# Optimization experiments

Measured on AMD Instinct MI355X. Metric: run time of the kernel, lower is better.

The kernel has to match this reference:

```python
import jax, jax.numpy as jnp
import numpy as np

EPS = 1e-12  # matches tf.math.l2_normalize epsilon used by K.l2_normalize


def setup_inputs() -> dict:
    key = jax.random.key(0)
    k1, k2, k3 = jax.random.split(key, 3)
    B, N, C = 512, 256, 256
    x = jax.random.normal(k1, (B, N, C), dtype=jnp.float32)
    kernel = jax.random.normal(k2, (N, 1), dtype=jnp.float32)
    bias = jax.random.normal(k3, (N,), dtype=jnp.float32)
    return {"x": x, "kernel": kernel, "bias": bias}


def reference(x, kernel, bias):
    # x: [B, N, C]; kernel: [N, 1]; bias: [N]
    N = x.shape[-2]
    mid = N // 2
    # self-similarity: [B, N, N]
    sim = jnp.einsum('bnc,bmc->bnm', x, x)
    # l2-normalize along last axis (tf semantics: x * rsqrt(max(sum(x^2), eps)))
    coe = sim * jax.lax.rsqrt(jnp.maximum(jnp.sum(sim * sim, axis=-1, keepdims=True), EPS))
    # center row scaled by kernel: [B, N, 1]
    coe0 = coe[:, mid, :][..., None] * kernel
    # gating logits: [B, N, 1]
    w = jnp.einsum('bnm,bmk->bnk', coe, coe0) + bias[None, :, None]
    # softmax over spatial axis N, broadcast-multiply with input
    return jax.nn.softmax(w, axis=-2) * x
```

## Files before the change

### kernel.cpp

```cpp
#include <hip/hip_runtime.h>

#define B_N 256
#define B_C 256
#define MID 128

typedef float f32x4 __attribute__((ext_vector_type(4)));
typedef __bf16 bf16x8 __attribute__((ext_vector_type(8)));
typedef short short8 __attribute__((ext_vector_type(8)));

__device__ __forceinline__ unsigned short f2bf(float f) {
  unsigned int u = __builtin_bit_cast(unsigned int, f);
  u += 0x7fffu + ((u >> 16) & 1u);
  return (unsigned short)(u >> 16);
}

__device__ __forceinline__ float bf2f(unsigned short h) {
  return __builtin_bit_cast(float, (unsigned int)h << 16);
}

__global__ __launch_bounds__(512, 2) void spat_attn(
    const float* __restrict__ x, const float* __restrict__ kern,
    const float* __restrict__ bias, float* __restrict__ out)
{
  __shared__ __align__(16) unsigned short Xs[B_N * B_C];
  __shared__ float smid[B_N];
  __shared__ float r2s[B_N];
  __shared__ float vb[B_N];
  __shared__ float wlog[B_N];
  __shared__ float wexp[B_N];

  const int b = blockIdx.x;
  const int tid = threadIdx.x;
  const float* __restrict__ xb = x + (size_t)b * (B_N * B_C);

  #pragma unroll 4
  for (int i = 0; i < 16; ++i) {
    const int e8 = i * 4096 + tid * 8;
    const float4 f0 = *reinterpret_cast<const float4*>(xb + e8);
    const float4 f1 = *reinterpret_cast<const float4*>(xb + e8 + 4);
    const int r = e8 >> 8;
    const int q = (e8 >> 3) & 31;
    union { unsigned short us[8]; short8 v; } P;
    P.us[0] = f2bf(f0.x); P.us[1] = f2bf(f0.y); P.us[2] = f2bf(f0.z); P.us[3] = f2bf(f0.w);
    P.us[4] = f2bf(f1.x); P.us[5] = f2bf(f1.y); P.us[6] = f2bf(f1.z); P.us[7] = f2bf(f1.w);
    *reinterpret_cast<short8*>(&Xs[(r << 8) + ((q ^ (r & 7)) << 3)]) = P.v;
  }
  __syncthreads();

  const int w  = tid >> 6;
  const int l  = tid & 63;
  const int lr = l & 15;
  const int g  = l >> 4;
  const int sw = lr & 7;

  f32x4 acc[16][2];
  #pragma unroll
  for (int t = 0; t < 16; ++t) {
    acc[t][0] = {0.f, 0.f, 0.f, 0.f};
    acc[t][1] = {0.f, 0.f, 0.f, 0.f};
  }

  const int rb0 = 32 * w + lr;
  const int rb1 = rb0 + 16;
  #pragma unroll
  for (int kk = 0; kk < 8; ++kk) {
    const int q  = 4 * kk + g;
    const int qs = ((q ^ sw) << 3);
    const bf16x8 b0 = __builtin_bit_cast(bf16x8,
        *reinterpret_cast<const short8*>(&Xs[(rb0 << 8) + qs]));
    const bf16x8 b1 = __builtin_bit_cast(bf16x8,
        *reinterpret_cast<const short8*>(&Xs[(rb1 << 8) + qs]));
    #pragma unroll
    for (int t = 0; t < 16; ++t) {
      const bf16x8 a = __builtin_bit_cast(bf16x8,
          *reinterpret_cast<const short8*>(&Xs[((16 * t + lr) << 8) + qs]));
      acc[t][0] = __builtin_amdgcn_mfma_f32_16x16x32_bf16(a, b0, acc[t][0], 0, 0, 0);
      acc[t][1] = __builtin_amdgcn_mfma_f32_16x16x32_bf16(a, b1, acc[t][1], 0, 0, 0);
    }
  }

  float rp0 = 0.f, rp1 = 0.f;
  #pragma unroll
  for (int t = 0; t < 16; ++t) {
    #pragma unroll
    for (int r = 0; r < 4; ++r) {
      rp0 += acc[t][0][r] * acc[t][0][r];
      rp1 += acc[t][1][r] * acc[t][1][r];
    }
  }
  rp0 += __shfl_xor(rp0, 16); rp0 += __shfl_xor(rp0, 32);
  rp1 += __shfl_xor(rp1, 16); rp1 += __shfl_xor(rp1, 32);
  if (l < 16) {
    r2s[32 * w + l]      = rp0;
    r2s[32 * w + 16 + l] = rp1;
    smid[32 * w + l]      = acc[8][0][0];
    smid[32 * w + 16 + l] = acc[8][1][0];
  }
  __syncthreads();

  if (tid < B_N) {
    const float rinvm = rsqrtf(fmaxf(r2s[MID], 1e-12f));
    vb[tid] = smid[tid] * rinvm * kern[tid];
  }
  __syncthreads();

  float up0 = 0.f, up1 = 0.f;
  #pragma unroll
  for (int t = 0; t < 16; ++t) {
    #pragma unroll
    for (int r = 0; r < 4; ++r) {
      const float vv = vb[16 * t + 4 * g + r];
      up0 += acc[t][0][r] * vv;
      up1 += acc[t][1][r] * vv;
    }
  }
  up0 += __shfl_xor(up0, 16); up0 += __shfl_xor(up0, 32);
  up1 += __shfl_xor(up1, 16); up1 += __shfl_xor(up1, 32);
  if (l < 16) {
    const int n0 = 32 * w + l, n1 = n0 + 16;
    wlog[n0] = up0 * rsqrtf(fmaxf(r2s[n0], 1e-12f)) + bias[n0];
    wlog[n1] = up1 * rsqrtf(fmaxf(r2s[n1], 1e-12f)) + bias[n1];
  }
  __syncthreads();

  if (tid < 64) {
    const float a0 = wlog[tid], a1 = wlog[tid + 64], a2 = wlog[tid + 128], a3 = wlog[tid + 192];
    float mx = fmaxf(fmaxf(a0, a1), fmaxf(a2, a3));
    #pragma unroll
    for (int off = 32; off >= 1; off >>= 1) mx = fmaxf(mx, __shfl_xor(mx, off));
    const float e0 = __expf(a0 - mx), e1 = __expf(a1 - mx), e2 = __expf(a2 - mx), e3 = __expf(a3 - mx);
    float s = e0 + e1 + e2 + e3;
    #pragma unroll
    for (int off = 32; off >= 1; off >>= 1) s += __shfl_xor(s, off);
    const float inv = 1.0f / s;
    wexp[tid] = e0 * inv; wexp[tid + 64] = e1 * inv;
    wexp[tid + 128] = e2 * inv; wexp[tid + 192] = e3 * inv;
  }
  __syncthreads();

  float* __restrict__ ob = out + (size_t)b * (B_N * B_C);
  #pragma unroll 4
  for (int i = 0; i < 16; ++i) {
    const int e8 = i * 4096 + tid * 8;
    const int r = e8 >> 8;
    const int q = (e8 >> 3) & 31;
    union { short8 v; unsigned short us[8]; } P;
    P.v = *reinterpret_cast<const short8*>(&Xs[(r << 8) + ((q ^ (r & 7)) << 3)]);
    const float wt = wexp[r];
    float4 o0, o1;
    o0.x = bf2f(P.us[0]) * wt; o0.y = bf2f(P.us[1]) * wt;
    o0.z = bf2f(P.us[2]) * wt; o0.w = bf2f(P.us[3]) * wt;
    o1.x = bf2f(P.us[4]) * wt; o1.y = bf2f(P.us[5]) * wt;
    o1.z = bf2f(P.us[6]) * wt; o1.w = bf2f(P.us[7]) * wt;
    *reinterpret_cast<float4*>(ob + e8)     = o0;
    *reinterpret_cast<float4*>(ob + e8 + 4) = o1;
  }
}

extern "C" void kernel_launch(void* const* d_in, const int* in_sizes, int n_in,
                              void* d_out, int out_size, void* d_ws, size_t ws_size,
                              hipStream_t stream) {
  const float* x    = (const float*)d_in[0];
  const float* kern = (const float*)d_in[1];
  const float* bias = (const float*)d_in[2];
  float* out = (float*)d_out;
  const int nb = in_sizes[0] / (B_N * B_C);
  spat_attn<<<dim3(nb), dim3(512), 0, stream>>>(x, kern, bias, out);
}
```

Before: 64.63 us.

## Process two batches per block and prefetch the second into registers

The grid is halved so each block handles two batch items. The second item's input is loaded into registers while the first item's output is stored, so the global load overlaps the store phase. Output stores become nontemporal and the bf16 conversion now uses the builtin cast. Each thread holds 32 extra float4 prefetch registers, which risks spills or lower occupancy under the 512x2 launch bound, and halving the grid to 256 blocks may leave compute units idle.

```diff
diff --git a/kernel.cpp b/kernel.cpp
--- a/kernel.cpp
+++ b/kernel.cpp
@@ -3,50 +3,34 @@
 #define B_N 256
 #define B_C 256
 #define MID 128
+#define NELEM (B_N * B_C)
 
 typedef float f32x4 __attribute__((ext_vector_type(4)));
 typedef __bf16 bf16x8 __attribute__((ext_vector_type(8)));
 typedef short short8 __attribute__((ext_vector_type(8)));
 
-__device__ __forceinline__ unsigned short f2bf(float f) {
-  unsigned int u = __builtin_bit_cast(unsigned int, f);
-  u += 0x7fffu + ((u >> 16) & 1u);
-  return (unsigned short)(u >> 16);
-}
-
 __device__ __forceinline__ float bf2f(unsigned short h) {
   return __builtin_bit_cast(float, (unsigned int)h << 16);
 }
 
-__global__ __launch_bounds__(512, 2) void spat_attn(
-    const float* __restrict__ x, const float* __restrict__ kern,
-    const float* __restrict__ bias, float* __restrict__ out)
-{
-  __shared__ __align__(16) unsigned short Xs[B_N * B_C];
-  __shared__ float smid[B_N];
-  __shared__ float r2s[B_N];
-  __shared__ float vb[B_N];
-  __shared__ float wlog[B_N];
-  __shared__ float wexp[B_N];
-
-  const int b = blockIdx.x;
-  const int tid = threadIdx.x;
-  const float* __restrict__ xb = x + (size_t)b * (B_N * B_C);
-
-  #pragma unroll 4
-  for (int i = 0; i < 16; ++i) {
-    const int e8 = i * 4096 + tid * 8;
-    const float4 f0 = *reinterpret_cast<const float4*>(xb + e8);
-    const float4 f1 = *reinterpret_cast<const float4*>(xb + e8 + 4);
-    const int r = e8 >> 8;
-    const int q = (e8 >> 3) & 31;
-    union { unsigned short us[8]; short8 v; } P;
-    P.us[0] = f2bf(f0.x); P.us[1] = f2bf(f0.y); P.us[2] = f2bf(f0.z); P.us[3] = f2bf(f0.w);
-    P.us[4] = f2bf(f1.x); P.us[5] = f2bf(f1.y); P.us[6] = f2bf(f1.z); P.us[7] = f2bf(f1.w);
-    *reinterpret_cast<short8*>(&Xs[(r << 8) + ((q ^ (r & 7)) << 3)]) = P.v;
-  }
-  __syncthreads();
-
+__device__ __forceinline__ short8 cvt8(float4 a, float4 b) {
+  union { unsigned short us[8]; short8 v; } P;
+  P.us[0] = __builtin_bit_cast(unsigned short, (__bf16)a.x);
+  P.us[1] = __builtin_bit_cast(unsigned short, (__bf16)a.y);
+  P.us[2] = __builtin_bit_cast(unsigned short, (__bf16)a.z);
+  P.us[3] = __builtin_bit_cast(unsigned short, (__bf16)a.w);
+  P.us[4] = __builtin_bit_cast(unsigned short, (__bf16)b.x);
+  P.us[5] = __builtin_bit_cast(unsigned short, (__bf16)b.y);
+  P.us[6] = __builtin_bit_cast(unsigned short, (__bf16)b.z);
+  P.us[7] = __builtin_bit_cast(unsigned short, (__bf16)b.w);
+  return P.v;
+}
+
+__device__ __forceinline__ void compute_batch(
+    const unsigned short* __restrict__ Xs, float* smid, float* r2s, float* vb,
+    float* wlog, float* wexp, const float* __restrict__ kern,
+    const float* __restrict__ bias, int tid)
+{
   const int w  = tid >> 6;
   const int l  = tid & 63;
   const int lr = l & 15;
@@ -137,8 +121,12 @@
     wexp[tid + 128] = e2 * inv; wexp[tid + 192] = e3 * inv;
   }
   __syncthreads();
-
-  float* __restrict__ ob = out + (size_t)b * (B_N * B_C);
+}
+
+__device__ __forceinline__ void store_out(
+    const unsigned short* __restrict__ Xs, const float* __restrict__ wexp,
+    float* __restrict__ ob, int tid)
+{
   #pragma unroll 4
   for (int i = 0; i < 16; ++i) {
     const int e8 = i * 4096 + tid * 8;
@@ -147,13 +135,76 @@
     union { short8 v; unsigned short us[8]; } P;
     P.v = *reinterpret_cast<const short8*>(&Xs[(r << 8) + ((q ^ (r & 7)) << 3)]);
     const float wt = wexp[r];
-    float4 o0, o1;
-    o0.x = bf2f(P.us[0]) * wt; o0.y = bf2f(P.us[1]) * wt;
-    o0.z = bf2f(P.us[2]) * wt; o0.w = bf2f(P.us[3]) * wt;
-    o1.x = bf2f(P.us[4]) * wt; o1.y = bf2f(P.us[5]) * wt;
-    o1.z = bf2f(P.us[6]) * wt; o1.w = bf2f(P.us[7]) * wt;
-    *reinterpret_cast<float4*>(ob + e8)     = o0;
-    *reinterpret_cast<float4*>(ob + e8 + 4) = o1;
+    f32x4 o0, o1;
+    o0[0] = bf2f(P.us[0]) * wt; o0[1] = bf2f(P.us[1]) * wt;
+    o0[2] = bf2f(P.us[2]) * wt; o0[3] = bf2f(P.us[3]) * wt;
+    o1[0] = bf2f(P.us[4]) * wt; o1[1] = bf2f(P.us[5]) * wt;
+    o1[2] = bf2f(P.us[6]) * wt; o1[3] = bf2f(P.us[7]) * wt;
+    __builtin_nontemporal_store(o0, reinterpret_cast<f32x4*>(ob + e8));
+    __builtin_nontemporal_store(o1, reinterpret_cast<f32x4*>(ob + e8 + 4));
+  }
+}
+
+__device__ __forceinline__ void lds_fill(
+    unsigned short* __restrict__ Xs, const float4* __restrict__ pf, int tid)
+{
+  #pragma unroll
+  for (int i = 0; i < 16; ++i) {
+    const int e8 = i * 4096 + tid * 8;
+    const int r = e8 >> 8;
+    const int q = (e8 >> 3) & 31;
+    *reinterpret_cast<short8*>(&Xs[(r << 8) + ((q ^ (r & 7)) << 3)]) =
+        cvt8(pf[2 * i], pf[2 * i + 1]);
+  }
+}
+
+__global__ __launch_bounds__(512, 2) void spat_attn(
+    const float* __restrict__ x, const float* __restrict__ kern,
+    const float* __restrict__ bias, float* __restrict__ out, int nb)
+{
+  __shared__ __align__(16) unsigned short Xs[NELEM];
+  __shared__ float smid[B_N];
+  __shared__ float r2s[B_N];
+  __shared__ float vb[B_N];
+  __shared__ float wlog[B_N];
+  __shared__ float wexp[B_N];
+
+  const int tid = threadIdx.x;
+  const int b0 = blockIdx.x;
+  const int b1 = blockIdx.x + gridDim.x;
+
+  {
+    const float* __restrict__ xb = x + (size_t)b0 * NELEM;
+    float4 pf0[32];
+    #pragma unroll
+    for (int i = 0; i < 16; ++i) {
+      pf0[2 * i]     = *reinterpret_cast<const float4*>(xb + i * 4096 + tid * 8);
+      pf0[2 * i + 1] = *reinterpret_cast<const float4*>(xb + i * 4096 + tid * 8 + 4);
+    }
+    lds_fill(Xs, pf0, tid);
+  }
+  __syncthreads();
+
+  compute_batch(Xs, smid, r2s, vb, wlog, wexp, kern, bias, tid);
+
+  const bool has2 = (b1 < nb);
+  float4 pf[32];
+  if (has2) {
+    const float* __restrict__ xb1 = x + (size_t)b1 * NELEM;
+    #pragma unroll
+    for (int i = 0; i < 16; ++i) {
+      pf[2 * i]     = *reinterpret_cast<const float4*>(xb1 + i * 4096 + tid * 8);
+      pf[2 * i + 1] = *reinterpret_cast<const float4*>(xb1 + i * 4096 + tid * 8 + 4);
+    }
+  }
+  store_out(Xs, wexp, out + (size_t)b0 * NELEM, tid);
+  __syncthreads();
+
+  if (has2) {
+    lds_fill(Xs, pf, tid);
+    __syncthreads();
+    compute_batch(Xs, smid, r2s, vb, wlog, wexp, kern, bias, tid);
+    store_out(Xs, wexp, out + (size_t)b1 * NELEM, tid);
   }
 }
 
@@ -164,6 +215,7 @@
   const float* kern = (const float*)d_in[1];
   const float* bias = (const float*)d_in[2];
   float* out = (float*)d_out;
-  const int nb = in_sizes[0] / (B_N * B_C);
-  spat_attn<<<dim3(nb), dim3(512), 0, stream>>>(x, kern, bias, out);
-}
+  const int nb = in_sizes[0] / NELEM;
+  const int grid = (nb + 1) / 2;
+  spat_attn<<<dim3(grid), dim3(512), 0, stream>>>(x, kern, bias, out, nb);
+}
```

Result: slower. 93.43 us (+44.6%).

## Pipeline global x loads in channel chunks overlapped with MFMA Gram computation

Applied to the files above, without the earlier changes.

Splits the load of x into four 64-channel chunks, with each thread loading half a row. The next chunk is prefetched into registers while MFMAs run on the current chunk, so global load latency overlaps the Gram matrix compute. It also switches to the native __bf16 conversion and relaxes launch_bounds to one block per CU, which allows more registers but may lower occupancy. The extra register buffer and three additional barriers add overhead.

```diff
diff --git a/kernel.cpp b/kernel.cpp
--- a/kernel.cpp
+++ b/kernel.cpp
@@ -3,55 +3,57 @@
 #define B_N 256
 #define B_C 256
 #define MID 128
+#define NELEM (B_N * B_C)
 
 typedef float f32x4 __attribute__((ext_vector_type(4)));
 typedef __bf16 bf16x8 __attribute__((ext_vector_type(8)));
 typedef short short8 __attribute__((ext_vector_type(8)));
 
-__device__ __forceinline__ unsigned short f2bf(float f) {
-  unsigned int u = __builtin_bit_cast(unsigned int, f);
-  u += 0x7fffu + ((u >> 16) & 1u);
-  return (unsigned short)(u >> 16);
-}
-
 __device__ __forceinline__ float bf2f(unsigned short h) {
   return __builtin_bit_cast(float, (unsigned int)h << 16);
 }
 
-__global__ __launch_bounds__(512, 2) void spat_attn(
+__device__ __forceinline__ short8 cvt8(float4 a, float4 b) {
+  union { unsigned short us[8]; short8 v; } P;
+  P.us[0] = __builtin_bit_cast(unsigned short, (__bf16)a.x);
+  P.us[1] = __builtin_bit_cast(unsigned short, (__bf16)a.y);
+  P.us[2] = __builtin_bit_cast(unsigned short, (__bf16)a.z);
+  P.us[3] = __builtin_bit_cast(unsigned short, (__bf16)a.w);
+  P.us[4] = __builtin_bit_cast(unsigned short, (__bf16)b.x);
+  P.us[5] = __builtin_bit_cast(unsigned short, (__bf16)b.y);
+  P.us[6] = __builtin_bit_cast(unsigned short, (__bf16)b.z);
+  P.us[7] = __builtin_bit_cast(unsigned short, (__bf16)b.w);
+  return P.v;
+}
+
+__global__ __launch_bounds__(512, 1) void spat_attn(
     const float* __restrict__ x, const float* __restrict__ kern,
     const float* __restrict__ bias, float* __restrict__ out)
 {
-  __shared__ __align__(16) unsigned short Xs[B_N * B_C];
+  __shared__ __align__(16) unsigned short Xs[NELEM];
   __shared__ float smid[B_N];
   __shared__ float r2s[B_N];
   __shared__ float vb[B_N];
   __shared__ float wlog[B_N];
   __shared__ float wexp[B_N];
 
+  const int tid = threadIdx.x;
   const int b = blockIdx.x;
-  const int tid = threadIdx.x;
-  const float* __restrict__ xb = x + (size_t)b * (B_N * B_C);
-
-  #pragma unroll 4
-  for (int i = 0; i < 16; ++i) {
-    const int e8 = i * 4096 + tid * 8;
-    const float4 f0 = *reinterpret_cast<const float4*>(xb + e8);
-    const float4 f1 = *reinterpret_cast<const float4*>(xb + e8 + 4);
-    const int r = e8 >> 8;
-    const int q = (e8 >> 3) & 31;
-    union { unsigned short us[8]; short8 v; } P;
-    P.us[0] = f2bf(f0.x); P.us[1] = f2bf(f0.y); P.us[2] = f2bf(f0.z); P.us[3] = f2bf(f0.w);
-    P.us[4] = f2bf(f1.x); P.us[5] = f2bf(f1.y); P.us[6] = f2bf(f1.z); P.us[7] = f2bf(f1.w);
-    *reinterpret_cast<short8*>(&Xs[(r << 8) + ((q ^ (r & 7)) << 3)]) = P.v;
-  }
-  __syncthreads();
+  const float* __restrict__ xb = x + (size_t)b * NELEM;
 
   const int w  = tid >> 6;
   const int l  = tid & 63;
   const int lr = l & 15;
   const int g  = l >> 4;
   const int sw = lr & 7;
+  const int rb0 = 32 * w + lr;
+  const int rb1 = rb0 + 16;
+
+  const int sr  = tid >> 1;
+  const int sh  = tid & 1;
+  const int srs = sr & 7;
+  const int sq0 = 4 * sh;
+  const float* __restrict__ sbase = xb + sr * B_C + sh * 32;
 
   f32x4 acc[16][2];
   #pragma unroll
@@ -60,22 +62,46 @@
     acc[t][1] = {0.f, 0.f, 0.f, 0.f};
   }
 
-  const int rb0 = 32 * w + lr;
-  const int rb1 = rb0 + 16;
+  float4 st[8];
+
   #pragma unroll
-  for (int kk = 0; kk < 8; ++kk) {
-    const int q  = 4 * kk + g;
-    const int qs = ((q ^ sw) << 3);
-    const bf16x8 b0 = __builtin_bit_cast(bf16x8,
-        *reinterpret_cast<const short8*>(&Xs[(rb0 << 8) + qs]));
-    const bf16x8 b1 = __builtin_bit_cast(bf16x8,
-        *reinterpret_cast<const short8*>(&Xs[(rb1 << 8) + qs]));
+  for (int j = 0; j < 8; ++j)
+    st[j] = *reinterpret_cast<const float4*>(sbase + 4 * j);
+  #pragma unroll
+  for (int m = 0; m < 4; ++m)
+    *reinterpret_cast<short8*>(&Xs[(sr << 8) + (((sq0 + m) ^ srs) << 3)]) =
+        cvt8(st[2 * m], st[2 * m + 1]);
+  __syncthreads();
+
+  #pragma unroll
+  for (int c = 0; c < 4; ++c) {
+    if (c < 3) {
+      #pragma unroll
+      for (int j = 0; j < 8; ++j)
+        st[j] = *reinterpret_cast<const float4*>(sbase + (c + 1) * 64 + 4 * j);
+    }
     #pragma unroll
-    for (int t = 0; t < 16; ++t) {
-      const bf16x8 a = __builtin_bit_cast(bf16x8,
-          *reinterpret_cast<const short8*>(&Xs[((16 * t + lr) << 8) + qs]));
-      acc[t][0] = __builtin_amdgcn_mfma_f32_16x16x32_bf16(a, b0, acc[t][0], 0, 0, 0);
-      acc[t][1] = __builtin_amdgcn_mfma_f32_16x16x32_bf16(a, b1, acc[t][1], 0, 0, 0);
+    for (int kk = 2 * c; kk < 2 * c + 2; ++kk) {
+      const int qs = (((4 * kk + g) ^ sw) << 3);
+      const bf16x8 bf0 = __builtin_bit_cast(bf16x8,
+          *reinterpret_cast<const short8*>(&Xs[(rb0 << 8) + qs]));
+      const bf16x8 bf1 = __builtin_bit_cast(bf16x8,
+          *reinterpret_cast<const short8*>(&Xs[(rb1 << 8) + qs]));
+      #pragma unroll
+      for (int t = 0; t < 16; ++t) {
+        const bf16x8 af = __builtin_bit_cast(bf16x8,
+            *reinterpret_cast<const short8*>(&Xs[((16 * t + lr) << 8) + qs]));
+        acc[t][0] = __builtin_amdgcn_mfma_f32_16x16x32_bf16(af, bf0, acc[t][0], 0, 0, 0);
+        acc[t][1] = __builtin_amdgcn_mfma_f32_16x16x32_bf16(af, bf1, acc[t][1], 0, 0, 0);
+      }
+    }
+    if (c < 3) {
+      #pragma unroll
+      for (int m = 0; m < 4; ++m)
+        *reinterpret_cast<short8*>(
+            &Xs[(sr << 8) + (((8 * (c + 1) + sq0 + m) ^ srs) << 3)]) =
+            cvt8(st[2 * m], st[2 * m + 1]);
+      __syncthreads();
     }
   }
 
@@ -138,7 +164,7 @@
   }
   __syncthreads();
 
-  float* __restrict__ ob = out + (size_t)b * (B_N * B_C);
+  float* __restrict__ ob = out + (size_t)b * NELEM;
   #pragma unroll 4
   for (int i = 0; i < 16; ++i) {
     const int e8 = i * 4096 + tid * 8;
@@ -147,13 +173,13 @@
     union { short8 v; unsigned short us[8]; } P;
     P.v = *reinterpret_cast<const short8*>(&Xs[(r << 8) + ((q ^ (r & 7)) << 3)]);
     const float wt = wexp[r];
-    float4 o0, o1;
-    o0.x = bf2f(P.us[0]) * wt; o0.y = bf2f(P.us[1]) * wt;
-    o0.z = bf2f(P.us[2]) * wt; o0.w = bf2f(P.us[3]) * wt;
-    o1.x = bf2f(P.us[4]) * wt; o1.y = bf2f(P.us[5]) * wt;
-    o1.z = bf2f(P.us[6]) * wt; o1.w = bf2f(P.us[7]) * wt;
-    *reinterpret_cast<float4*>(ob + e8)     = o0;
-    *reinterpret_cast<float4*>(ob + e8 + 4) = o1;
+    f32x4 o0, o1;
+    o0[0] = bf2f(P.us[0]) * wt; o0[1] = bf2f(P.us[1]) * wt;
+    o0[2] = bf2f(P.us[2]) * wt; o0[3] = bf2f(P.us[3]) * wt;
+    o1[0] = bf2f(P.us[4]) * wt; o1[1] = bf2f(P.us[5]) * wt;
+    o1[2] = bf2f(P.us[6]) * wt; o1[3] = bf2f(P.us[7]) * wt;
+    *reinterpret_cast<f32x4*>(ob + e8)     = o0;
+    *reinterpret_cast<f32x4*>(ob + e8 + 4) = o1;
   }
 }
 
@@ -164,6 +190,6 @@
   const float* kern = (const float*)d_in[1];
   const float* bias = (const float*)d_in[2];
   float* out = (float*)d_out;
-  const int nb = in_sizes[0] / (B_N * B_C);
+  const int nb = in_sizes[0] / NELEM;
   spat_attn<<<dim3(nb), dim3(512), 0, stream>>>(x, kern, bias, out);
 }
```

After: 70.91 us. 9.7% more time.
